# Optimization experiments

Hardware: AMD Instinct MI355X
Metric: run time of the kernel (lower is better)

## Reference

```python
import jax, jax.numpy as jnp
import numpy as np

T, M = 64, 64
ROI, SPA, WORD, I3D = 2048, 4, 300, 1024
H, D = 512, 256  # so_hidden, so_out_dim (= rel_dim)
IN = ROI + SPA + WORD  # 2352


def _w(k, shape):
    return jax.random.normal(k, shape, dtype=jnp.float32) * 0.02


def setup_inputs() -> dict:
    key = jax.random.key(0)
    ks = jax.random.split(key, 32)
    inp = {
        "roi_feats": jax.random.normal(ks[0], (T, M, ROI), dtype=jnp.float32),
        "spatial": jax.random.uniform(ks[1], (T, M, SPA), dtype=jnp.float32),
        "i3d_feats": jax.random.normal(ks[2], (T, I3D), dtype=jnp.float32),
        "subj_emb": jax.random.normal(ks[3], (WORD,), dtype=jnp.float32),
        "obj_emb": jax.random.normal(ks[4], (WORD,), dtype=jnp.float32),
        "pred_emb": jax.random.normal(ks[5], (WORD,), dtype=jnp.float32),
        # subject / object encoders (torch Linear convention: W is (out,in))
        "subj_w1": _w(ks[6], (H, IN)), "subj_b1": _w(ks[7], (H,)),
        "subj_w2": _w(ks[8], (D, H)), "subj_b2": _w(ks[9], (D,)),
        "obj_w1": _w(ks[10], (H, IN)), "obj_b1": _w(ks[11], (H,)),
        "obj_w2": _w(ks[12], (D, H)), "obj_b2": _w(ks[13], (D,)),
        # fuse MLPs (in = 2*D)
        "fuse_s_w1": _w(ks[14], (H, 2 * D)), "fuse_s_b1": _w(ks[15], (H,)),
        "fuse_s_w2": _w(ks[16], (D, H)), "fuse_s_b2": _w(ks[17], (D,)),
        "fuse_o_w1": _w(ks[18], (H, 2 * D)), "fuse_o_b1": _w(ks[19], (H,)),
        "fuse_o_w2": _w(ks[20], (D, H)), "fuse_o_b2": _w(ks[21], (D,)),
        # relation projections + MLP
        "W_rs": _w(ks[22], (D, D)),
        "W_ro": _w(ks[23], (D, D)),
        "rel_w1": _w(ks[24], (H, D + WORD)), "rel_b1": _w(ks[25], (H,)),
        "rel_w2": _w(ks[26], (D, H)), "rel_b2": _w(ks[27], (D,)),
    }
    return inp


def _linear(x, W, b):
    return x @ W.T + b


def _mlp2(x, w1, b1, w2, b2):
    return _linear(jax.nn.relu(_linear(x, w1, b1)), w2, b2)


def reference(roi_feats, spatial, i3d_feats, subj_emb, obj_emb, pred_emb,
              subj_w1, subj_b1, subj_w2, subj_b2,
              obj_w1, obj_b1, obj_w2, obj_b2,
              fuse_s_w1, fuse_s_b1, fuse_s_w2, fuse_s_b2,
              fuse_o_w1, fuse_o_b1, fuse_o_w2, fuse_o_b2,
              W_rs, W_ro, rel_w1, rel_b1, rel_w2, rel_b2):
    Tn, Mn, _ = roi_feats.shape
    se = jnp.broadcast_to(subj_emb, (Tn, Mn, subj_emb.shape[-1]))
    oe = jnp.broadcast_to(obj_emb, (Tn, Mn, obj_emb.shape[-1]))
    # SubjectObjectEncoder: fc2(relu(fc1([roi; spa; word])))
    fs_base = _mlp2(jnp.concatenate([roi_feats, spatial, se], axis=-1),
                    subj_w1, subj_b1, subj_w2, subj_b2)  # (T,M,D)
    fo_base = _mlp2(jnp.concatenate([roi_feats, spatial, oe], axis=-1),
                    obj_w1, obj_b1, obj_w2, obj_b2)
    # use_gsa = use_lla = False -> fuse([base; base])
    fs = _mlp2(jnp.concatenate([fs_base, fs_base], axis=-1),
               fuse_s_w1, fuse_s_b1, fuse_s_w2, fuse_s_b2)
    fo = _mlp2(jnp.concatenate([fo_base, fo_base], axis=-1),
               fuse_o_w1, fuse_o_b1, fuse_o_w2, fuse_o_b2)
    # Eq. 15: pairwise diff + predicate word, then 2-layer MLP
    fs_proj = fs @ W_rs.T
    fo_proj = fo @ W_ro.T
    diff = fs_proj[:, :, None, :] - fo_proj[:, None, :, :]  # (T,M,M,D)
    # rel_fc1([diff; pred]) split into diff part + constant pred part
    Wd, Wp = rel_w1[:, :fs.shape[-1]], rel_w1[:, fs.shape[-1]:]
    h = jax.nn.relu(diff @ Wd.T + (pred_emb @ Wp.T + rel_b1))  # (T,M,M,H)
    return h @ rel_w2.T + rel_b2  # (T,M,M,D)
```

## Files before the change

kernel.cpp:

```cpp
#include <hip/hip_runtime.h>
#include <hip/hip_bf16.h>

typedef __attribute__((ext_vector_type(4))) float f32x4;
typedef __attribute__((ext_vector_type(8))) short s16x8;

__device__ __forceinline__ void async_lds16(const void* g, void* l) {
  __builtin_amdgcn_global_load_lds((const __attribute__((address_space(1))) void*)g,
                                   (__attribute__((address_space(3))) void*)l, 16, 0, 0);
}

__device__ __forceinline__ short f2bf(float x) {
  __hip_bfloat16 h = __float2bfloat16(x);
  short s;
  __builtin_memcpy(&s, &h, 2);
  return s;
}

__device__ __forceinline__ s16x8 pack8(f32x4 a, f32x4 b) {
  s16x8 r;
  r[0] = f2bf(a[0]); r[1] = f2bf(a[1]); r[2] = f2bf(a[2]); r[3] = f2bf(a[3]);
  r[4] = f2bf(b[0]); r[5] = f2bf(b[1]); r[6] = f2bf(b[2]); r[7] = f2bf(b[3]);
  return r;
}

template<bool RELU, bool OUT_BF16, bool HAS_BIAS>
__global__ __launch_bounds__(256) void gemm_bt(
    const __hip_bfloat16* __restrict__ Ag, const __hip_bfloat16* __restrict__ Bg,
    const float* __restrict__ biasg, void* __restrict__ Cg,
    int lda, int ldb, int K, int ldc,
    int strideA, int strideB, int strideBias, long strideC)
{
  __shared__ __align__(16) short As[4096];
  __shared__ __align__(16) short Bs[4096];
  const int tid  = threadIdx.x;
  const int lane = tid & 63;
  const int wid  = tid >> 6;
  const int z    = blockIdx.z;
  const __hip_bfloat16* A = Ag + (long)z * strideA;
  const __hip_bfloat16* B = Bg + (long)z * strideB;
  const float* bias = HAS_BIAS ? (biasg + (long)z * strideBias) : nullptr;
  const int row0 = blockIdx.y * 128;
  const int col0 = blockIdx.x * 128;

  const int srow = wid * 16 + (lane >> 2);
  const int scol = (lane & 3) * 8;

  f32x4 acc[4][4];
#pragma unroll
  for (int i = 0; i < 4; ++i)
#pragma unroll
    for (int j = 0; j < 4; ++j) acc[i][j] = (f32x4)(0.0f);

  const int rw = (wid & 1) * 64;
  const int cw = (wid >> 1) * 64;
  const int lm = lane & 15;
  const int kg = (lane >> 4) * 8;

  for (int ks = 0; ks < K; ks += 32) {
    __syncthreads();
#pragma unroll
    for (int is = 0; is < 2; ++is) {
      async_lds16(A + (long)(row0 + is * 64 + srow) * lda + ks + scol,
                  (char*)As + is * 4096 + wid * 1024);
      async_lds16(B + (long)(col0 + is * 64 + srow) * ldb + ks + scol,
                  (char*)Bs + is * 4096 + wid * 1024);
    }
    __syncthreads();
    s16x8 af[4], bf[4];
#pragma unroll
    for (int mt = 0; mt < 4; ++mt)
      af[mt] = *(const s16x8*)(As + (rw + mt * 16 + lm) * 32 + kg);
#pragma unroll
    for (int nt = 0; nt < 4; ++nt)
      bf[nt] = *(const s16x8*)(Bs + (cw + nt * 16 + lm) * 32 + kg);
#pragma unroll
    for (int mt = 0; mt < 4; ++mt)
#pragma unroll
      for (int nt = 0; nt < 4; ++nt)
        acc[mt][nt] = __builtin_amdgcn_mfma_f32_16x16x32_bf16(af[mt], bf[nt], acc[mt][nt], 0, 0, 0);
  }

  const int lr4 = (lane >> 4) * 4;
#pragma unroll
  for (int mt = 0; mt < 4; ++mt) {
#pragma unroll
    for (int nt = 0; nt < 4; ++nt) {
      const int col = col0 + cw + nt * 16 + lm;
      const float bv = HAS_BIAS ? bias[col] : 0.0f;
#pragma unroll
      for (int r = 0; r < 4; ++r) {
        const int row = row0 + rw + mt * 16 + lr4 + r;
        float v = acc[mt][nt][r] + bv;
        if (RELU) v = fmaxf(v, 0.0f);
        if (OUT_BF16)
          ((__hip_bfloat16*)Cg)[(long)z * strideC + (long)row * ldc + col] = __float2bfloat16(v);
        else
          ((float*)Cg)[(long)z * strideC + (long)row * ldc + col] = v;
      }
    }
  }
}

template<bool RELU, bool OUT_BF16, bool HAS_BIAS>
__global__ __launch_bounds__(256) void gemm_bt64(
    const __hip_bfloat16* __restrict__ Ag, const __hip_bfloat16* __restrict__ Bg,
    const float* __restrict__ biasg, void* __restrict__ Cg,
    int lda, int ldb, int K, int ldc,
    int strideA, int strideB, int strideBias, long strideC)
{
  __shared__ __align__(16) short As[2048];
  __shared__ __align__(16) short Bs[2048];
  const int tid  = threadIdx.x;
  const int lane = tid & 63;
  const int wid  = tid >> 6;
  const int z    = blockIdx.z;
  const __hip_bfloat16* A = Ag + (long)z * strideA;
  const __hip_bfloat16* B = Bg + (long)z * strideB;
  const float* bias = HAS_BIAS ? (biasg + (long)z * strideBias) : nullptr;
  const int row0 = blockIdx.y * 64;
  const int col0 = blockIdx.x * 64;

  const int srow = wid * 16 + (lane >> 2);
  const int scol = (lane & 3) * 8;

  f32x4 acc[2][2];
#pragma unroll
  for (int i = 0; i < 2; ++i)
#pragma unroll
    for (int j = 0; j < 2; ++j) acc[i][j] = (f32x4)(0.0f);

  const int rw = (wid & 1) * 32;
  const int cw = (wid >> 1) * 32;
  const int lm = lane & 15;
  const int kg = (lane >> 4) * 8;

  for (int ks = 0; ks < K; ks += 32) {
    __syncthreads();
    async_lds16(A + (long)(row0 + srow) * lda + ks + scol, (char*)As + wid * 1024);
    async_lds16(B + (long)(col0 + srow) * ldb + ks + scol, (char*)Bs + wid * 1024);
    __syncthreads();
    s16x8 af[2], bf[2];
#pragma unroll
    for (int mt = 0; mt < 2; ++mt)
      af[mt] = *(const s16x8*)(As + (rw + mt * 16 + lm) * 32 + kg);
#pragma unroll
    for (int nt = 0; nt < 2; ++nt)
      bf[nt] = *(const s16x8*)(Bs + (cw + nt * 16 + lm) * 32 + kg);
#pragma unroll
    for (int mt = 0; mt < 2; ++mt)
#pragma unroll
      for (int nt = 0; nt < 2; ++nt)
        acc[mt][nt] = __builtin_amdgcn_mfma_f32_16x16x32_bf16(af[mt], bf[nt], acc[mt][nt], 0, 0, 0);
  }

  const int lr4 = (lane >> 4) * 4;
#pragma unroll
  for (int mt = 0; mt < 2; ++mt) {
#pragma unroll
    for (int nt = 0; nt < 2; ++nt) {
      const int col = col0 + cw + nt * 16 + lm;
      const float bv = HAS_BIAS ? bias[col] : 0.0f;
#pragma unroll
      for (int r = 0; r < 4; ++r) {
        const int row = row0 + rw + mt * 16 + lr4 + r;
        float v = acc[mt][nt][r] + bv;
        if (RELU) v = fmaxf(v, 0.0f);
        if (OUT_BF16)
          ((__hip_bfloat16*)Cg)[(long)z * strideC + (long)row * ldc + col] = __float2bfloat16(v);
        else
          ((float*)Cg)[(long)z * strideC + (long)row * ldc + col] = v;
      }
    }
  }
}

__global__ __launch_bounds__(256) void reduce_relu(
    const float* __restrict__ P, const float* __restrict__ cboth,
    __hip_bfloat16* __restrict__ H1)
{
  const int id = blockIdx.x * 256 + threadIdx.x;
  const int row = id >> 7, c8 = id & 127;
  const f32x4* p0 = (const f32x4*)(P + (long)row * 1024 + c8 * 8);
  const f32x4* p1 = (const f32x4*)(P + 4194304 + (long)row * 1024 + c8 * 8);
  const f32x4* bb = (const f32x4*)(cboth + c8 * 8);
  f32x4 a = p0[0] + p1[0] + bb[0];
  f32x4 b = p0[1] + p1[1] + bb[1];
#pragma unroll
  for (int e = 0; e < 4; ++e) { a[e] = fmaxf(a[e], 0.0f); b[e] = fmaxf(b[e], 0.0f); }
  *(s16x8*)((short*)H1 + (long)row * 1024 + c8 * 8) = pack8(a, b);
}

__global__ __launch_bounds__(256, 4) void rel_final(
    const float* __restrict__ AsBo, const __hip_bfloat16* __restrict__ W2b,
    const float* __restrict__ b2, float* __restrict__ out)
{
  __shared__ __align__(16) short Ws[2][8192];
  __shared__ __align__(16) short Hs[2][2048];
  const int tid  = threadIdx.x;
  const int lane = tid & 63;
  const int wid  = tid >> 6;
  const int bid = (int)blockIdx.x;
  const int swz = (bid & 7) * 512 + (bid >> 3);
  const int t = swz >> 6;
  const int i = swz & 63;

  const float* Ap = AsBo + (long)(t * 64 + i) * 512;
  const float* Bp = AsBo + 2097152 + (long)t * 64 * 512;

  const int lm   = lane & 15;
  const int kgrp = lane >> 4;

  const int fj  = tid >> 2;
  const int fks = tid & 3;
  const float* fb = Bp + fj * 512 + fks * 8;
  const float* fa = Ap + fks * 8;
  const int hw = fj * 64 + ((fks ^ ((fj >> 1) & 3)) << 4);

  const char* w2src = (const char*)W2b
      + (long)(wid * 64 + (lane >> 2)) * 1024
      + ((((lane & 3) ^ ((lane >> 3) & 3))) << 4);

  const int fslot = (kgrp ^ ((lm >> 1) & 3)) << 4;

  f32x4 acc[4][4];
#pragma unroll
  for (int a = 0; a < 4; ++a)
#pragma unroll
    for (int b = 0; b < 4; ++b) acc[a][b] = (f32x4)(0.0f);

  {
#pragma unroll
    for (int q = 0; q < 4; ++q)
      async_lds16(w2src + q * 16384, (char*)Ws[0] + wid * 4096 + q * 1024);
    f32x4 b0 = *(const f32x4*)(fb);
    f32x4 b1 = *(const f32x4*)(fb + 4);
    f32x4 a0 = *(const f32x4*)(fa);
    f32x4 a1 = *(const f32x4*)(fa + 4);
    f32x4 d0, d1;
#pragma unroll
    for (int e = 0; e < 4; ++e) {
      d0[e] = fmaxf(a0[e] - b0[e], 0.0f);
      d1[e] = fmaxf(a1[e] - b1[e], 0.0f);
    }
    *(s16x8*)((char*)Hs[0] + hw) = pack8(d0, d1);
  }
  __syncthreads();

#pragma unroll
  for (int ch = 0; ch < 16; ++ch) {
    const int cur = ch & 1;
    s16x8 af[4], bf[4];
#pragma unroll
    for (int mt = 0; mt < 4; ++mt)
      af[mt] = *(const s16x8*)((char*)Hs[cur] + (mt * 16 + lm) * 64 + fslot);
#pragma unroll
    for (int nt = 0; nt < 4; ++nt)
      bf[nt] = *(const s16x8*)((char*)Ws[cur] + wid * 4096 + nt * 1024
                               + lm * 64 + fslot);
    f32x4 av0, av1, bv0, bv1;
    if (ch < 15) {
      const int ko = (ch + 1) * 32;
      bv0 = *(const f32x4*)(fb + ko);
      bv1 = *(const f32x4*)(fb + ko + 4);
      av0 = *(const f32x4*)(fa + ko);
      av1 = *(const f32x4*)(fa + ko + 4);
#pragma unroll
      for (int q = 0; q < 4; ++q)
        async_lds16(w2src + (ch + 1) * 64 + q * 16384,
                    (char*)Ws[cur ^ 1] + wid * 4096 + q * 1024);
    }
    __builtin_amdgcn_s_setprio(1);
#pragma unroll
    for (int mt = 0; mt < 4; ++mt)
#pragma unroll
      for (int nt = 0; nt < 4; ++nt)
        acc[mt][nt] = __builtin_amdgcn_mfma_f32_16x16x32_bf16(
            af[mt], bf[nt], acc[mt][nt], 0, 0, 0);
    __builtin_amdgcn_s_setprio(0);
    if (ch < 15) {
      f32x4 d0, d1;
#pragma unroll
      for (int e = 0; e < 4; ++e) {
        d0[e] = fmaxf(av0[e] - bv0[e], 0.0f);
        d1[e] = fmaxf(av1[e] - bv1[e], 0.0f);
      }
      *(s16x8*)((char*)Hs[cur ^ 1] + hw) = pack8(d0, d1);
    }
    __syncthreads();
  }

  const long obase = (long)(t * 64 + i) * 16384;
#pragma unroll
  for (int mt = 0; mt < 4; ++mt) {
#pragma unroll
    for (int nt = 0; nt < 4; ++nt) {
      const int col = wid * 64 + nt * 16 + lm;
      const float bvv = b2[col];
#pragma unroll
      for (int r = 0; r < 4; ++r) {
        const int j = mt * 16 + kgrp * 4 + r;
        out[obase + j * 256 + col] = acc[mt][nt][r] + bvv;
      }
    }
  }
}

__global__ __launch_bounds__(256) void prep_kernel(
    const float* __restrict__ roi, const float* __restrict__ spatial,
    const float* __restrict__ subj_emb, const float* __restrict__ obj_emb,
    const float* __restrict__ pred_emb,
    const float* __restrict__ subj_w1, const float* __restrict__ subj_b1,
    const float* __restrict__ obj_w1, const float* __restrict__ obj_b1,
    const float* __restrict__ subj_w2, const float* __restrict__ subj_b2,
    const float* __restrict__ obj_w2, const float* __restrict__ obj_b2,
    const float* __restrict__ fs_w1, const float* __restrict__ fs_b1,
    const float* __restrict__ fs_w2, const float* __restrict__ fs_b2,
    const float* __restrict__ fo_w1, const float* __restrict__ fo_b1,
    const float* __restrict__ fo_w2, const float* __restrict__ fo_b2,
    const float* __restrict__ W_rs, const float* __restrict__ W_ro,
    const float* __restrict__ rel_w1, const float* __restrict__ rel_b1,
    const float* __restrict__ rel_w2,
    __hip_bfloat16* __restrict__ XP, __hip_bfloat16* __restrict__ W1P,
    float* __restrict__ cboth,
    __hip_bfloat16* __restrict__ Bcat2, float* __restrict__ bias2,
    __hip_bfloat16* __restrict__ WfCat, float* __restrict__ biasf,
    __hip_bfloat16* __restrict__ W4cat, float* __restrict__ bias4,
    __hip_bfloat16* __restrict__ WcCat, float* __restrict__ crel,
    __hip_bfloat16* __restrict__ W2b)
{
  int id = blockIdx.x * 256 + threadIdx.x;

  if (id < 1081344) {
    int row = id / 264, c8 = id - row * 264;
    s16x8 o;
    if (c8 < 256) {
      const f32x4* src = (const f32x4*)(roi + (long)row * 2048 + c8 * 8);
      o = pack8(src[0], src[1]);
    } else {
      f32x4 a, b;
#pragma unroll
      for (int e = 0; e < 4; ++e) {
        int col = c8 * 8 + e;
        a[e] = (col < 2052) ? spatial[row * 4 + (col - 2048)] : 0.0f;
        int col2 = col + 4;
        b[e] = (col2 < 2052) ? spatial[row * 4 + (col2 - 2048)] : 0.0f;
      }
      o = pack8(a, b);
    }
    *(s16x8*)((short*)XP + (long)id * 8) = o;
    return;
  }
  id -= 1081344;
  if (id < 270336) {
    int row = id / 264, c8 = id - row * 264;
    const float* w = (row < 512) ? (subj_w1 + (long)row * 2352)
                                 : (obj_w1 + (long)(row - 512) * 2352);
    s16x8 o;
    if (c8 < 256) {
      const f32x4* src = (const f32x4*)(w + c8 * 8);
      o = pack8(src[0], src[1]);
    } else {
      f32x4 a, b;
#pragma unroll
      for (int e = 0; e < 4; ++e) {
        int col = c8 * 8 + e;
        a[e] = (col < 2052) ? w[col] : 0.0f;
        int col2 = col + 4;
        b[e] = (col2 < 2052) ? w[col2] : 0.0f;
      }
      o = pack8(a, b);
    }
    *(s16x8*)((short*)W1P + (long)id * 8) = o;
    return;
  }
  id -= 270336;
  if (id < 1024) {
    int h = id;
    const float* w; const float* e; float s;
    if (h < 512) { w = subj_w1 + (long)h * 2352 + 2052; e = subj_emb; s = subj_b1[h]; }
    else { w = obj_w1 + (long)(h - 512) * 2352 + 2052; e = obj_emb; s = obj_b1[h - 512]; }
    for (int k = 0; k < 300; ++k) s += w[k] * e[k];
    cboth[h] = s;
    return;
  }
  id -= 1024;
  if (id < 32768) {
    const float* src = (id < 16384) ? (subj_w2 + id * 8) : (obj_w2 + (id - 16384) * 8);
    const f32x4* s4 = (const f32x4*)src;
    *(s16x8*)((short*)Bcat2 + (long)id * 8) = pack8(s4[0], s4[1]);
    return;
  }
  id -= 32768;
  if (id < 512) { bias2[id] = (id < 256) ? subj_b2[id] : obj_b2[id - 256]; return; }
  id -= 512;
  if (id < 32768) {
    int z = id >> 14, r8 = id & 16383;
    int h = r8 >> 5, d8 = r8 & 31;
    const float* w = (z ? fo_w1 : fs_w1) + h * 512 + d8 * 8;
    const f32x4* lo = (const f32x4*)w;
    const f32x4* hi = (const f32x4*)(w + 256);
    *(s16x8*)((short*)WfCat + (long)id * 8) = pack8(lo[0] + hi[0], lo[1] + hi[1]);
    return;
  }
  id -= 32768;
  if (id < 1024) { biasf[id] = (id < 512) ? fs_b1[id] : fo_b1[id - 512]; return; }
  id -= 1024;
  if (id < 32768) {
    const float* src = (id < 16384) ? (fs_w2 + id * 8) : (fo_w2 + (id - 16384) * 8);
    const f32x4* s4 = (const f32x4*)src;
    *(s16x8*)((short*)W4cat + (long)id * 8) = pack8(s4[0], s4[1]);
    return;
  }
  id -= 32768;
  if (id < 512) { bias4[id] = (id < 256) ? fs_b2[id] : fo_b2[id - 256]; return; }
  id -= 512;
  if (id < 262144) {
    int z = id >> 17, r = id & 131071;
    int h = r >> 8, d = r & 255;
    const float* Wr = z ? W_ro : W_rs;
    const float* wd = rel_w1 + (long)h * 556;
    float s = 0.0f;
    for (int e = 0; e < 256; ++e) s += wd[e] * Wr[e * 256 + d];
    WcCat[id] = __float2bfloat16(s);
    return;
  }
  id -= 262144;
  if (id < 1024) {
    int z = id >> 9, h = id & 511;
    float s = 0.0f;
    if (z == 0) {
      s = rel_b1[h];
      const float* wp = rel_w1 + (long)h * 556 + 256;
      for (int k = 0; k < 300; ++k) s += pred_emb[k] * wp[k];
    }
    crel[id] = s;
    return;
  }
  id -= 1024;
  if (id < 16384) {
    const f32x4* s4 = (const f32x4*)(rel_w2 + id * 8);
    *(s16x8*)((short*)W2b + (long)id * 8) = pack8(s4[0], s4[1]);
  }
}

extern "C" void kernel_launch(void* const* d_in, const int* in_sizes, int n_in,
                              void* d_out, int out_size, void* d_ws, size_t ws_size,
                              hipStream_t stream)
{
  const float* roi       = (const float*)d_in[0];
  const float* spatial   = (const float*)d_in[1];
  const float* subj_emb  = (const float*)d_in[3];
  const float* obj_emb   = (const float*)d_in[4];
  const float* pred_emb  = (const float*)d_in[5];
  const float* subj_w1   = (const float*)d_in[6];
  const float* subj_b1   = (const float*)d_in[7];
  const float* subj_w2   = (const float*)d_in[8];
  const float* subj_b2   = (const float*)d_in[9];
  const float* obj_w1    = (const float*)d_in[10];
  const float* obj_b1    = (const float*)d_in[11];
  const float* obj_w2    = (const float*)d_in[12];
  const float* obj_b2    = (const float*)d_in[13];
  const float* fuse_s_w1 = (const float*)d_in[14];
  const float* fuse_s_b1 = (const float*)d_in[15];
  const float* fuse_s_w2 = (const float*)d_in[16];
  const float* fuse_s_b2 = (const float*)d_in[17];
  const float* fuse_o_w1 = (const float*)d_in[18];
  const float* fuse_o_b1 = (const float*)d_in[19];
  const float* fuse_o_w2 = (const float*)d_in[20];
  const float* fuse_o_b2 = (const float*)d_in[21];
  const float* W_rs      = (const float*)d_in[22];
  const float* W_ro      = (const float*)d_in[23];
  const float* rel_w1    = (const float*)d_in[24];
  const float* rel_b1    = (const float*)d_in[25];
  const float* rel_w2    = (const float*)d_in[26];
  const float* rel_b2    = (const float*)d_in[27];

  char* ws = (char*)d_ws;
  __hip_bfloat16* XP   = (__hip_bfloat16*)(ws);
  float*          AsBo = (float*)(ws);
  __hip_bfloat16* W1P  = (__hip_bfloat16*)(ws + 17301504);
  __hip_bfloat16* H1   = (__hip_bfloat16*)(ws + 21626880);
  __hip_bfloat16* FS   = (__hip_bfloat16*)(ws + 30015488);
  float*          P    = (float*)(ws + 34209792);
  const size_t so = 67764224;
  __hip_bfloat16* Bcat2 = (__hip_bfloat16*)(ws + so);
  float*          bias2 = (float*)(ws + so + 524288);
  __hip_bfloat16* WfCat = (__hip_bfloat16*)(ws + so + 526336);
  float*          biasf = (float*)(ws + so + 1050624);
  __hip_bfloat16* W4cat = (__hip_bfloat16*)(ws + so + 1054720);
  float*          bias4 = (float*)(ws + so + 1579008);
  __hip_bfloat16* WcCat = (__hip_bfloat16*)(ws + so + 1581056);
  float*          crel  = (float*)(ws + so + 2105344);
  __hip_bfloat16* W2b   = (__hip_bfloat16*)(ws + so + 2109440);
  float*          cboth = (float*)(ws + so + 2371584);

  prep_kernel<<<6768, 256, 0, stream>>>(
      roi, spatial, subj_emb, obj_emb, pred_emb,
      subj_w1, subj_b1, obj_w1, obj_b1, subj_w2, subj_b2, obj_w2, obj_b2,
      fuse_s_w1, fuse_s_b1, fuse_s_w2, fuse_s_b2,
      fuse_o_w1, fuse_o_b1, fuse_o_w2, fuse_o_b2,
      W_rs, W_ro, rel_w1, rel_b1, rel_w2,
      XP, W1P, cboth, Bcat2, bias2, WfCat, biasf, W4cat, bias4, WcCat, crel, W2b);

  gemm_bt<false, false, false><<<dim3(8, 32, 2), 256, 0, stream>>>(
      XP, W1P, cboth, P, 2112, 2112, 1056, 1024, 1056, 1056, 0, 4194304L);
  reduce_relu<<<2048, 256, 0, stream>>>(P, cboth, H1);
  gemm_bt64<false, true, true><<<dim3(4, 64, 2), 256, 0, stream>>>(
      H1, Bcat2, bias2, FS, 1024, 512, 512, 512, 512, 131072, 256, 256);
  gemm_bt64<true, true, true><<<dim3(8, 64, 2), 256, 0, stream>>>(
      FS, WfCat, biasf, H1, 512, 256, 256, 1024, 256, 131072, 512, 512);
  gemm_bt64<false, true, true><<<dim3(4, 64, 2), 256, 0, stream>>>(
      H1, W4cat, bias4, FS, 1024, 512, 512, 512, 512, 131072, 256, 256);
  gemm_bt64<false, false, true><<<dim3(8, 64, 2), 256, 0, stream>>>(
      FS, WcCat, crel, AsBo, 512, 256, 256, 512, 256, 131072, 512, 2097152L);
  rel_final<<<4096, 256, 0, stream>>>(AsBo, W2b, rel_b2, (float*)d_out);
}
```

Baseline: 529.6 us.

## Double-buffer LDS tiles in GEMM kernels to overlap loads with MFMA

```diff
diff --git a/kernel.cpp b/kernel.cpp
--- a/kernel.cpp
+++ b/kernel.cpp
@@ -30,8 +30,8 @@
     int lda, int ldb, int K, int ldc,
     int strideA, int strideB, int strideBias, long strideC)
 {
-  __shared__ __align__(16) short As[4096];
-  __shared__ __align__(16) short Bs[4096];
+  __shared__ __align__(16) short As[2][4096];
+  __shared__ __align__(16) short Bs[2][4096];
   const int tid  = threadIdx.x;
   const int lane = tid & 63;
   const int wid  = tid >> 6;
@@ -55,29 +55,44 @@
   const int cw = (wid >> 1) * 64;
   const int lm = lane & 15;
   const int kg = (lane >> 4) * 8;
-
-  for (int ks = 0; ks < K; ks += 32) {
-    __syncthreads();
-#pragma unroll
-    for (int is = 0; is < 2; ++is) {
-      async_lds16(A + (long)(row0 + is * 64 + srow) * lda + ks + scol,
-                  (char*)As + is * 4096 + wid * 1024);
-      async_lds16(B + (long)(col0 + is * 64 + srow) * ldb + ks + scol,
-                  (char*)Bs + is * 4096 + wid * 1024);
-    }
-    __syncthreads();
+  const int nk = K >> 5;
+
+#pragma unroll
+  for (int is = 0; is < 2; ++is) {
+    async_lds16(A + (long)(row0 + is * 64 + srow) * lda + scol,
+                (char*)As[0] + is * 4096 + wid * 1024);
+    async_lds16(B + (long)(col0 + is * 64 + srow) * ldb + scol,
+                (char*)Bs[0] + is * 4096 + wid * 1024);
+  }
+  __syncthreads();
+
+  for (int it = 0; it < nk; ++it) {
+    const int cur = it & 1;
+    if (it + 1 < nk) {
+      const int ksn = (it + 1) << 5;
+#pragma unroll
+      for (int is = 0; is < 2; ++is) {
+        async_lds16(A + (long)(row0 + is * 64 + srow) * lda + ksn + scol,
+                    (char*)As[cur ^ 1] + is * 4096 + wid * 1024);
+        async_lds16(B + (long)(col0 + is * 64 + srow) * ldb + ksn + scol,
+                    (char*)Bs[cur ^ 1] + is * 4096 + wid * 1024);
+      }
+    }
     s16x8 af[4], bf[4];
 #pragma unroll
     for (int mt = 0; mt < 4; ++mt)
-      af[mt] = *(const s16x8*)(As + (rw + mt * 16 + lm) * 32 + kg);
+      af[mt] = *(const s16x8*)(As[cur] + (rw + mt * 16 + lm) * 32 + kg);
 #pragma unroll
     for (int nt = 0; nt < 4; ++nt)
-      bf[nt] = *(const s16x8*)(Bs + (cw + nt * 16 + lm) * 32 + kg);
+      bf[nt] = *(const s16x8*)(Bs[cur] + (cw + nt * 16 + lm) * 32 + kg);
+    __builtin_amdgcn_s_setprio(1);
 #pragma unroll
     for (int mt = 0; mt < 4; ++mt)
 #pragma unroll
       for (int nt = 0; nt < 4; ++nt)
         acc[mt][nt] = __builtin_amdgcn_mfma_f32_16x16x32_bf16(af[mt], bf[nt], acc[mt][nt], 0, 0, 0);
+    __builtin_amdgcn_s_setprio(0);
+    __syncthreads();
   }
 
   const int lr4 = (lane >> 4) * 4;
@@ -108,8 +123,8 @@
     int lda, int ldb, int K, int ldc,
     int strideA, int strideB, int strideBias, long strideC)
 {
-  __shared__ __align__(16) short As[2048];
-  __shared__ __align__(16) short Bs[2048];
+  __shared__ __align__(16) short As[2][2048];
+  __shared__ __align__(16) short Bs[2][2048];
   const int tid  = threadIdx.x;
   const int lane = tid & 63;
   const int wid  = tid >> 6;
@@ -133,24 +148,36 @@
   const int cw = (wid >> 1) * 32;
   const int lm = lane & 15;
   const int kg = (lane >> 4) * 8;
-
-  for (int ks = 0; ks < K; ks += 32) {
-    __syncthreads();
-    async_lds16(A + (long)(row0 + srow) * lda + ks + scol, (char*)As + wid * 1024);
-    async_lds16(B + (long)(col0 + srow) * ldb + ks + scol, (char*)Bs + wid * 1024);
-    __syncthreads();
+  const int nk = K >> 5;
+
+  async_lds16(A + (long)(row0 + srow) * lda + scol, (char*)As[0] + wid * 1024);
+  async_lds16(B + (long)(col0 + srow) * ldb + scol, (char*)Bs[0] + wid * 1024);
+  __syncthreads();
+
+  for (int it = 0; it < nk; ++it) {
+    const int cur = it & 1;
+    if (it + 1 < nk) {
+      const int ksn = (it + 1) << 5;
+      async_lds16(A + (long)(row0 + srow) * lda + ksn + scol,
+                  (char*)As[cur ^ 1] + wid * 1024);
+      async_lds16(B + (long)(col0 + srow) * ldb + ksn + scol,
+                  (char*)Bs[cur ^ 1] + wid * 1024);
+    }
     s16x8 af[2], bf[2];
 #pragma unroll
     for (int mt = 0; mt < 2; ++mt)
-      af[mt] = *(const s16x8*)(As + (rw + mt * 16 + lm) * 32 + kg);
+      af[mt] = *(const s16x8*)(As[cur] + (rw + mt * 16 + lm) * 32 + kg);
 #pragma unroll
     for (int nt = 0; nt < 2; ++nt)
-      bf[nt] = *(const s16x8*)(Bs + (cw + nt * 16 + lm) * 32 + kg);
+      bf[nt] = *(const s16x8*)(Bs[cur] + (cw + nt * 16 + lm) * 32 + kg);
+    __builtin_amdgcn_s_setprio(1);
 #pragma unroll
     for (int mt = 0; mt < 2; ++mt)
 #pragma unroll
       for (int nt = 0; nt < 2; ++nt)
         acc[mt][nt] = __builtin_amdgcn_mfma_f32_16x16x32_bf16(af[mt], bf[nt], acc[mt][nt], 0, 0, 0);
+    __builtin_amdgcn_s_setprio(0);
+    __syncthreads();
   }
 
   const int lr4 = (lane >> 4) * 4;
```

Measured after the change: 528.2 us. No clear change (-0.3%).
